# Optimization experiments

Hardware: AMD Instinct MI355X
Metric: run time of the kernel (lower is better)

The kernel has to match this reference:

```python
import jax, jax.numpy as jnp
import numpy as np

B, M, K, D = 16384, 16, 256, 64
T = 1.0


def setup_inputs() -> dict:
    key = jax.random.key(0)
    k1, k2 = jax.random.split(key)
    x = jax.random.normal(k1, (B, M, D), dtype=jnp.float32)
    # nn.init.normal_(self.center, std=0.01)
    center = jax.random.normal(k2, (M, K, D), dtype=jnp.float32) * 0.01
    return {"x": x, "center": center}


def _forward(x, center):
    # x: [B, M, D]; center: [M, K, D]
    x1 = jax.lax.stop_gradient(x)              # x.detach() in the original
    x_sqlen = jnp.sum(x1 * x1, axis=-1)        # [B, M]
    dot = jnp.einsum('mkd,bmd->bmk', center, x1)  # bmm(center, x1) -> [B, M, K]
    c_sqlen = jnp.sum(center * center, axis=-1)   # [M, K]
    dist = c_sqlen[None, :, :] - 2.0 * dot + x_sqlen[:, :, None]  # [B, M, K]
    dist = -jnp.sqrt(dist)
    # softargmax with straight-through estimator
    y_soft = jax.nn.softmax(dist / T, axis=-1)
    label = jnp.argmax(y_soft, axis=-1, keepdims=True)            # [B, M, 1]
    y_hard = jax.nn.one_hot(label[..., 0], K, dtype=dist.dtype)   # [B, M, K]
    assign = y_hard - jax.lax.stop_gradient(y_soft) + y_soft
    # reconstruction: bmm(assign^T(M,B,K), center(M,K,D)) -> [B, M, D]
    recon = jnp.einsum('bmk,mkd->bmd', assign, center)
    return recon, center, label


def reference(x, center):
    return _forward(x, center)
```

## Files before the change

### kernel.cpp

```cpp
#include <hip/hip_runtime.h>
#include <stdint.h>
#include <math.h>

#define B_TOT 16384
#define M_TOT 16
#define K_TOT 256
#define D_TOT 64
#define ROWS_PB 256
#define THREADS 512
#define NCHUNK (B_TOT / ROWS_PB)
#define CAP 2048
#define XERRF 0.0160f
#define CBIG  0.22f
#define SLACK 5.0e-5f

typedef unsigned long long ull;
typedef __attribute__((ext_vector_type(8))) short short8;
typedef __attribute__((ext_vector_type(4))) float f32x4;
typedef __attribute__((ext_vector_type(4))) uint32_t u32x4;

__device__ __forceinline__ uint32_t f32_key(float f) {
  uint32_t u = __float_as_uint(f);
  return (u & 0x80000000u) ? ~u : (u | 0x80000000u);
}
__device__ __forceinline__ ull u64min(ull a, ull b) { return a < b ? a : b; }

__device__ __forceinline__ uint32_t bf16rne(float f) {
  uint32_t u = __float_as_uint(f);
  return (u + 0x7FFFu + ((u >> 16) & 1u)) >> 16;
}
__device__ __forceinline__ uint32_t pack2(float a, float b) {
  return bf16rne(a) | (bf16rne(b) << 16);
}

__device__ __forceinline__ int swz(int row, int c) {
  return row * 128 + ((c * 16) ^ ((row & 7) << 4));
}

#define XLA_SUM64_LANE16(RES, P)                                      \
  do {                                                                \
    float _r[16];                                                     \
    _Pragma("unroll") for (int _j = 0; _j < 16; ++_j) _r[_j] = P(_j); \
    _Pragma("unroll") for (int _mm = 1; _mm < 4; ++_mm)               \
      _Pragma("unroll") for (int _j = 0; _j < 16; ++_j) {             \
        float _q = P(16 * _mm + _j);                                  \
        _r[_j] = _r[_j] + _q;                                         \
      }                                                               \
    float _u[8];                                                      \
    _Pragma("unroll") for (int _j = 0; _j < 8; ++_j) _u[_j] = _r[_j] + _r[_j + 8]; \
    float _v[4];                                                      \
    _Pragma("unroll") for (int _j = 0; _j < 4; ++_j) _v[_j] = _u[_j] + _u[_j + 4]; \
    float _w0 = _v[0] + _v[2];                                        \
    float _w1 = _v[1] + _v[3];                                        \
    RES = _w0 + _w1;                                                  \
  } while (0)

__device__ __forceinline__ ull exact_key_stream(int k, const float* __restrict__ xrow,
                                                const float* __restrict__ crow,
                                                float csq, float x_sq) {
#pragma clang fp contract(off)
#pragma clang fp reassociate(off)
  const float4* cp = reinterpret_cast<const float4*>(crow);
  const float4* xp = reinterpret_cast<const float4*>(xrow);
  float a[4] = {0.f, 0.f, 0.f, 0.f};
#pragma unroll
  for (int it = 0; it < 4; ++it) {
    float cc[16], xx[16];
#pragma unroll
    for (int q = 0; q < 4; ++q) {
      float4 v = cp[4 * it + q];
      cc[4 * q + 0] = v.x; cc[4 * q + 1] = v.y;
      cc[4 * q + 2] = v.z; cc[4 * q + 3] = v.w;
      float4 w = xp[4 * it + q];
      xx[4 * q + 0] = w.x; xx[4 * q + 1] = w.y;
      xx[4 * q + 2] = w.z; xx[4 * q + 3] = w.w;
    }
#pragma unroll
    for (int L = 0; L < 4; ++L) {
      float m3 = cc[12 + L] * xx[12 + L];
      float s3 = m3 + a[L];
      float m2 = cc[8 + L] * xx[8 + L];
      float s2 = m2 + s3;
      float m1 = cc[4 + L] * xx[4 + L];
      float s1 = m1 + s2;
      float m0 = cc[0 + L] * xx[0 + L];
      a[L] = m0 + s1;
    }
  }
  const float dot = (a[0] + a[1]) + (a[2] + a[3]);
  const float two_dot = 2.0f * dot;
  const float d2 = (csq - two_dot) + x_sq;
  const float s = (float)sqrt((double)d2);
  return (((ull)f32_key(s)) << 32) | (unsigned)k;
}

__global__ __launch_bounds__(THREADS, 4) void mkmeans_fwd(
    const float* __restrict__ x, const float* __restrict__ center,
    float* __restrict__ recon, float* __restrict__ outC, float* __restrict__ outL)
{
#pragma clang fp contract(off)
#pragma clang fp reassociate(off)
  __shared__ __align__(16) char s_xb[ROWS_PB * 128];
  __shared__ __align__(16) char s_cb[K_TOT * 128];
  __shared__ __align__(16) float s_csq[K_TOT];
  __shared__ __align__(16) float s_csqrt[K_TOT];
  __shared__ float s_xsq[ROWS_PB];
  __shared__ float s_xnorm[ROWS_PB];
  __shared__ ull s_best[ROWS_PB];
  __shared__ uint32_t s_list[CAP];
  __shared__ int s_nc, s_ovf;

  const int t = threadIdx.x;
  const int l = t & 63;
  const int wv = t >> 6;
  const int g = l >> 4;
  const int j = l & 15;
  const int bi = blockIdx.x;
  const int m = bi & (M_TOT - 1);
  const int chunk = bi >> 4;
  const int b0 = chunk * ROWS_PB;

  const float* cmbase = center + (size_t)m * (K_TOT * D_TOT);

  if (t == 0) { s_nc = 0; s_ovf = 0; }

  if (t < ROWS_PB) {
    const float4* xp = reinterpret_cast<const float4*>(
        x + ((size_t)((b0 + t) * M_TOT + m)) * D_TOT);
    float xf[64];
#pragma unroll
    for (int i = 0; i < 16; ++i) {
      float4 v = xp[i];
      xf[4 * i + 0] = v.x; xf[4 * i + 1] = v.y;
      xf[4 * i + 2] = v.z; xf[4 * i + 3] = v.w;
    }
    float xsq;
#define PX(I) (xf[(I)] * xf[(I)])
    XLA_SUM64_LANE16(xsq, PX);
#undef PX
    s_xsq[t] = xsq;
    s_xnorm[t] = sqrtf(xsq) * 1.00001f + 1e-12f;
#pragma unroll
    for (int c = 0; c < 8; ++c) {
      u32x4 u = {pack2(xf[8 * c + 0], xf[8 * c + 1]),
                 pack2(xf[8 * c + 2], xf[8 * c + 3]),
                 pack2(xf[8 * c + 4], xf[8 * c + 5]),
                 pack2(xf[8 * c + 6], xf[8 * c + 7])};
      *reinterpret_cast<u32x4*>(s_xb + swz(t, c)) = u;
    }
    s_best[t] = ~0ull;
  } else {
    const int tc = t - ROWS_PB;
    const float4* cp = reinterpret_cast<const float4*>(cmbase + (size_t)tc * D_TOT);
    float cf[64];
#pragma unroll
    for (int i = 0; i < 16; ++i) {
      float4 v = cp[i];
      cf[4 * i + 0] = v.x; cf[4 * i + 1] = v.y;
      cf[4 * i + 2] = v.z; cf[4 * i + 3] = v.w;
    }
    float csq;
#define PC(I) (cf[(I)] * cf[(I)])
    XLA_SUM64_LANE16(csq, PC);
#undef PC
    s_csq[tc] = csq;
    s_csqrt[tc] = sqrtf(csq) * 1.00001f + 1e-12f;
#pragma unroll
    for (int c = 0; c < 8; ++c) {
      u32x4 u = {pack2(cf[8 * c + 0], cf[8 * c + 1]),
                 pack2(cf[8 * c + 2], cf[8 * c + 3]),
                 pack2(cf[8 * c + 4], cf[8 * c + 5]),
                 pack2(cf[8 * c + 6], cf[8 * c + 7])};
      *reinterpret_cast<u32x4*>(s_cb + swz(tc, c)) = u;
    }
    if (chunk == 0) {
      float4* dst = reinterpret_cast<float4*>(
          outC + (size_t)m * (K_TOT * D_TOT) + (size_t)tc * D_TOT);
#pragma unroll
      for (int i = 0; i < 16; ++i)
        dst[i] = *reinterpret_cast<const float4*>(&cf[4 * i]);
    }
  }
  __syncthreads();

  const int row0 = wv * 32 + j;
  const int row1 = row0 + 16;
  short8 bfr[2][2];
  float xnorm[2];
#pragma unroll
  for (int rg = 0; rg < 2; ++rg) {
    const int row = rg ? row1 : row0;
#pragma unroll
    for (int ks = 0; ks < 2; ++ks)
      bfr[rg][ks] = *reinterpret_cast<const short8*>(s_xb + swz(row, ks * 4 + g));
    xnorm[rg] = s_xnorm[row];
  }

  float m1[2] = {3.0e38f, 3.0e38f};
#pragma unroll
  for (int T = 0; T < 16; ++T) {
    short8 af[2];
#pragma unroll
    for (int ks = 0; ks < 2; ++ks)
      af[ks] = *reinterpret_cast<const short8*>(s_cb + swz(T * 16 + j, ks * 4 + g));
    const f32x4 cq = *reinterpret_cast<const f32x4*>(&s_csq[T * 16 + g * 4]);
#pragma unroll
    for (int rg = 0; rg < 2; ++rg) {
      f32x4 a = {0.f, 0.f, 0.f, 0.f};
      a = __builtin_amdgcn_mfma_f32_16x16x32_bf16(af[0], bfr[rg][0], a, 0, 0, 0);
      a = __builtin_amdgcn_mfma_f32_16x16x32_bf16(af[1], bfr[rg][1], a, 0, 0, 0);
      const float e0 = fmaf(-2.0f, a[0], cq[0]);
      const float e1 = fmaf(-2.0f, a[1], cq[1]);
      const float e2 = fmaf(-2.0f, a[2], cq[2]);
      const float e3 = fmaf(-2.0f, a[3], cq[3]);
      m1[rg] = fminf(m1[rg], fminf(fminf(e0, e1), fminf(e2, e3)));
    }
  }
  float mthr[2], xbb[2];
#pragma unroll
  for (int rg = 0; rg < 2; ++rg) {
    float v = m1[rg];
    v = fminf(v, __shfl_xor(v, 16, 64));
    v = fminf(v, __shfl_xor(v, 32, 64));
    xbb[rg] = XERRF * xnorm[rg];
    mthr[rg] = v + xbb[rg] * CBIG + SLACK;
  }

#pragma unroll
  for (int T = 0; T < 16; ++T) {
    short8 af[2];
#pragma unroll
    for (int ks = 0; ks < 2; ++ks)
      af[ks] = *reinterpret_cast<const short8*>(s_cb + swz(T * 16 + j, ks * 4 + g));
    const f32x4 cq = *reinterpret_cast<const f32x4*>(&s_csq[T * 16 + g * 4]);
    const f32x4 cs = *reinterpret_cast<const f32x4*>(&s_csqrt[T * 16 + g * 4]);
#pragma unroll
    for (int rg = 0; rg < 2; ++rg) {
      f32x4 a = {0.f, 0.f, 0.f, 0.f};
      a = __builtin_amdgcn_mfma_f32_16x16x32_bf16(af[0], bfr[rg][0], a, 0, 0, 0);
      a = __builtin_amdgcn_mfma_f32_16x16x32_bf16(af[1], bfr[rg][1], a, 0, 0, 0);
      const int row = rg ? row1 : row0;
#pragma unroll
      for (int i = 0; i < 4; ++i) {
        const float am = fmaf(-2.0f, a[i], cq[i]);
        const float thr = fmaf(xbb[rg], cs[i], mthr[rg]);
        if (am <= thr) {
          const int idx = atomicAdd(&s_nc, 1);
          if (idx < CAP)
            s_list[idx] = ((uint32_t)row << 16) | (uint32_t)(T * 16 + g * 4 + i);
          else
            s_ovf = 1;
        }
      }
    }
  }
  __syncthreads();

  if (!s_ovf) {
    const int n = s_nc;
#pragma unroll 1
    for (int i = t; i < n; i += THREADS) {
      const uint32_t e = s_list[i];
      const int row = (int)(e >> 16);
      const int k = (int)(e & 0xffffu);
      const float* xrow = x + ((size_t)((b0 + row) * M_TOT + m)) * D_TOT;
      const float* crow = cmbase + (size_t)k * D_TOT;
      const ull key = exact_key_stream(k, xrow, crow, s_csq[k], s_xsq[row]);
      atomicMin(&s_best[row], key);
    }
  } else if (t < ROWS_PB) {
    const float* xrow = x + ((size_t)((b0 + t) * M_TOT + m)) * D_TOT;
    ull best = ~0ull;
#pragma unroll 1
    for (int k = 0; k < K_TOT; ++k)
      best = u64min(best, exact_key_stream(k, xrow, cmbase + (size_t)k * D_TOT,
                                           s_csq[k], s_xsq[t]));
    s_best[t] = best;
  }
  __syncthreads();

  if (t < ROWS_PB)
    outL[(size_t)(b0 + t) * M_TOT + m] = (float)(uint32_t)(s_best[t] & 0xffffffffull);

  const float4* cm4 = reinterpret_cast<const float4*>(cmbase);
  float4* rec4 = reinterpret_cast<float4*>(recon);
#pragma unroll
  for (int it = 0; it < (ROWS_PB * 16) / THREADS; ++it) {
    const int slot = it * THREADS + t;
    const int row = slot >> 4, ch = slot & 15;
    const int kst = (int)(s_best[row] & 0xffffffffull);
    rec4[((size_t)((b0 + row) * M_TOT + m)) * 16 + ch] = cm4[kst * 16 + ch];
  }
}

extern "C" void kernel_launch(void* const* d_in, const int* in_sizes, int n_in,
                              void* d_out, int out_size, void* d_ws, size_t ws_size,
                              hipStream_t stream) {
  const float* x = (const float*)d_in[0];
  const float* center = (const float*)d_in[1];
  float* recon = (float*)d_out;
  float* outC = recon + (size_t)B_TOT * M_TOT * D_TOT;
  float* outL = outC + (size_t)M_TOT * K_TOT * D_TOT;

  mkmeans_fwd<<<dim3(NCHUNK * M_TOT), dim3(THREADS), 0, stream>>>(x, center, recon, outC, outL);
}
```

Measured before the change: 172.5 us.

## Fuse two MFMA passes into one with online max and candidate bitmasks

Replaces the two-pass candidate search, which ran the bf16 MFMA distance computation twice (once for the minimum, once to collect candidates), with a single pass. That pass seeds the MFMA accumulator with -0.5*||c||^2, tracks a running maximum, and records candidate bits per lane in a 64-bit mask that is reset whenever the maximum jumps. The per-center error bound becomes a uniform bound using the maximum center norm for the block. Staging of x and centers is also restructured to stream in chunks and fuse the outC copy. The looser uniform bound may admit more candidates into the exact rescoring list.

```diff
diff --git a/kernel.cpp b/kernel.cpp
--- a/kernel.cpp
+++ b/kernel.cpp
@@ -11,7 +11,6 @@
 #define NCHUNK (B_TOT / ROWS_PB)
 #define CAP 2048
 #define XERRF 0.0160f
-#define CBIG  0.22f
 #define SLACK 5.0e-5f
 
 typedef unsigned long long ull;
@@ -37,23 +36,19 @@
   return row * 128 + ((c * 16) ^ ((row & 7) << 4));
 }
 
-#define XLA_SUM64_LANE16(RES, P)                                      \
-  do {                                                                \
-    float _r[16];                                                     \
-    _Pragma("unroll") for (int _j = 0; _j < 16; ++_j) _r[_j] = P(_j); \
-    _Pragma("unroll") for (int _mm = 1; _mm < 4; ++_mm)               \
-      _Pragma("unroll") for (int _j = 0; _j < 16; ++_j) {             \
-        float _q = P(16 * _mm + _j);                                  \
-        _r[_j] = _r[_j] + _q;                                         \
-      }                                                               \
-    float _u[8];                                                      \
-    _Pragma("unroll") for (int _j = 0; _j < 8; ++_j) _u[_j] = _r[_j] + _r[_j + 8]; \
-    float _v[4];                                                      \
-    _Pragma("unroll") for (int _j = 0; _j < 4; ++_j) _v[_j] = _u[_j] + _u[_j + 4]; \
-    float _w0 = _v[0] + _v[2];                                        \
-    float _w1 = _v[1] + _v[3];                                        \
-    RES = _w0 + _w1;                                                  \
-  } while (0)
+__device__ __forceinline__ float xla_hsum16(const float* r) {
+#pragma clang fp contract(off)
+#pragma clang fp reassociate(off)
+  float u[8];
+#pragma unroll
+  for (int q = 0; q < 8; ++q) u[q] = r[q] + r[q + 8];
+  float v[4];
+#pragma unroll
+  for (int q = 0; q < 4; ++q) v[q] = u[q] + u[q + 4];
+  float w0 = v[0] + v[2];
+  float w1 = v[1] + v[3];
+  return w0 + w1;
+}
 
 __device__ __forceinline__ ull exact_key_stream(int k, const float* __restrict__ xrow,
                                                 const float* __restrict__ crow,
@@ -103,9 +98,10 @@
   __shared__ __align__(16) char s_xb[ROWS_PB * 128];
   __shared__ __align__(16) char s_cb[K_TOT * 128];
   __shared__ __align__(16) float s_csq[K_TOT];
-  __shared__ __align__(16) float s_csqrt[K_TOT];
+  __shared__ __align__(16) float s_nch[K_TOT];
   __shared__ float s_xsq[ROWS_PB];
   __shared__ float s_xnorm[ROWS_PB];
+  __shared__ float s_cmaxw[4];
   __shared__ ull s_best[ROWS_PB];
   __shared__ uint32_t s_list[CAP];
   __shared__ int s_nc, s_ovf;
@@ -127,130 +123,134 @@
   if (t < ROWS_PB) {
     const float4* xp = reinterpret_cast<const float4*>(
         x + ((size_t)((b0 + t) * M_TOT + m)) * D_TOT);
-    float xf[64];
-#pragma unroll
-    for (int i = 0; i < 16; ++i) {
-      float4 v = xp[i];
-      xf[4 * i + 0] = v.x; xf[4 * i + 1] = v.y;
-      xf[4 * i + 2] = v.z; xf[4 * i + 3] = v.w;
-    }
-    float xsq;
-#define PX(I) (xf[(I)] * xf[(I)])
-    XLA_SUM64_LANE16(xsq, PX);
-#undef PX
+    float r[16];
+#pragma unroll
+    for (int mm = 0; mm < 4; ++mm) {
+      float q[16];
+#pragma unroll
+      for (int qq = 0; qq < 4; ++qq) {
+        float4 v = xp[4 * mm + qq];
+        q[4 * qq + 0] = v.x; q[4 * qq + 1] = v.y;
+        q[4 * qq + 2] = v.z; q[4 * qq + 3] = v.w;
+      }
+#pragma unroll
+      for (int jj = 0; jj < 16; ++jj) {
+        const float p = q[jj] * q[jj];
+        r[jj] = (mm == 0) ? p : (r[jj] + p);
+      }
+#pragma unroll
+      for (int h = 0; h < 2; ++h) {
+        u32x4 u = {pack2(q[8 * h + 0], q[8 * h + 1]),
+                   pack2(q[8 * h + 2], q[8 * h + 3]),
+                   pack2(q[8 * h + 4], q[8 * h + 5]),
+                   pack2(q[8 * h + 6], q[8 * h + 7])};
+        *reinterpret_cast<u32x4*>(s_xb + swz(t, 2 * mm + h)) = u;
+      }
+    }
+    const float xsq = xla_hsum16(r);
     s_xsq[t] = xsq;
     s_xnorm[t] = sqrtf(xsq) * 1.00001f + 1e-12f;
-#pragma unroll
-    for (int c = 0; c < 8; ++c) {
-      u32x4 u = {pack2(xf[8 * c + 0], xf[8 * c + 1]),
-                 pack2(xf[8 * c + 2], xf[8 * c + 3]),
-                 pack2(xf[8 * c + 4], xf[8 * c + 5]),
-                 pack2(xf[8 * c + 6], xf[8 * c + 7])};
-      *reinterpret_cast<u32x4*>(s_xb + swz(t, c)) = u;
-    }
     s_best[t] = ~0ull;
   } else {
     const int tc = t - ROWS_PB;
     const float4* cp = reinterpret_cast<const float4*>(cmbase + (size_t)tc * D_TOT);
-    float cf[64];
-#pragma unroll
-    for (int i = 0; i < 16; ++i) {
-      float4 v = cp[i];
-      cf[4 * i + 0] = v.x; cf[4 * i + 1] = v.y;
-      cf[4 * i + 2] = v.z; cf[4 * i + 3] = v.w;
-    }
-    float csq;
-#define PC(I) (cf[(I)] * cf[(I)])
-    XLA_SUM64_LANE16(csq, PC);
-#undef PC
+    float4* dst = (chunk == 0)
+        ? reinterpret_cast<float4*>(outC + (size_t)m * (K_TOT * D_TOT) + (size_t)tc * D_TOT)
+        : nullptr;
+    float r[16];
+#pragma unroll
+    for (int mm = 0; mm < 4; ++mm) {
+      float q[16];
+#pragma unroll
+      for (int qq = 0; qq < 4; ++qq) {
+        float4 v = cp[4 * mm + qq];
+        if (dst) dst[4 * mm + qq] = v;
+        q[4 * qq + 0] = v.x; q[4 * qq + 1] = v.y;
+        q[4 * qq + 2] = v.z; q[4 * qq + 3] = v.w;
+      }
+#pragma unroll
+      for (int jj = 0; jj < 16; ++jj) {
+        const float p = q[jj] * q[jj];
+        r[jj] = (mm == 0) ? p : (r[jj] + p);
+      }
+#pragma unroll
+      for (int h = 0; h < 2; ++h) {
+        u32x4 u = {pack2(q[8 * h + 0], q[8 * h + 1]),
+                   pack2(q[8 * h + 2], q[8 * h + 3]),
+                   pack2(q[8 * h + 4], q[8 * h + 5]),
+                   pack2(q[8 * h + 6], q[8 * h + 7])};
+        *reinterpret_cast<u32x4*>(s_cb + swz(tc, 2 * mm + h)) = u;
+      }
+    }
+    const float csq = xla_hsum16(r);
     s_csq[tc] = csq;
-    s_csqrt[tc] = sqrtf(csq) * 1.00001f + 1e-12f;
-#pragma unroll
-    for (int c = 0; c < 8; ++c) {
-      u32x4 u = {pack2(cf[8 * c + 0], cf[8 * c + 1]),
-                 pack2(cf[8 * c + 2], cf[8 * c + 3]),
-                 pack2(cf[8 * c + 4], cf[8 * c + 5]),
-                 pack2(cf[8 * c + 6], cf[8 * c + 7])};
-      *reinterpret_cast<u32x4*>(s_cb + swz(tc, c)) = u;
-    }
-    if (chunk == 0) {
-      float4* dst = reinterpret_cast<float4*>(
-          outC + (size_t)m * (K_TOT * D_TOT) + (size_t)tc * D_TOT);
-#pragma unroll
-      for (int i = 0; i < 16; ++i)
-        dst[i] = *reinterpret_cast<const float4*>(&cf[4 * i]);
-    }
+    s_nch[tc] = -0.5f * csq;
+    float cs = sqrtf(csq) * 1.00001f + 1e-12f;
+#pragma unroll
+    for (int off = 1; off < 64; off <<= 1)
+      cs = fmaxf(cs, __shfl_xor(cs, off, 64));
+    if (l == 0) s_cmaxw[wv - 4] = cs;
   }
   __syncthreads();
 
   const int row0 = wv * 32 + j;
   const int row1 = row0 + 16;
   short8 bfr[2][2];
-  float xnorm[2];
 #pragma unroll
   for (int rg = 0; rg < 2; ++rg) {
     const int row = rg ? row1 : row0;
 #pragma unroll
     for (int ks = 0; ks < 2; ++ks)
       bfr[rg][ks] = *reinterpret_cast<const short8*>(s_xb + swz(row, ks * 4 + g));
-    xnorm[rg] = s_xnorm[row];
-  }
-
-  float m1[2] = {3.0e38f, 3.0e38f};
+  }
+  const float cmax = fmaxf(fmaxf(s_cmaxw[0], s_cmaxw[1]),
+                           fmaxf(s_cmaxw[2], s_cmaxw[3]));
+  float Wa[2];
+  Wa[0] = XERRF * s_xnorm[row0] * cmax + 0.5f * SLACK;
+  Wa[1] = XERRF * s_xnorm[row1] * cmax + 0.5f * SLACK;
+
+  float m1[2] = {-3.0e38f, -3.0e38f};
+  ull mk[2] = {0ull, 0ull};
 #pragma unroll
   for (int T = 0; T < 16; ++T) {
-    short8 af[2];
-#pragma unroll
-    for (int ks = 0; ks < 2; ++ks)
-      af[ks] = *reinterpret_cast<const short8*>(s_cb + swz(T * 16 + j, ks * 4 + g));
-    const f32x4 cq = *reinterpret_cast<const f32x4*>(&s_csq[T * 16 + g * 4]);
+    short8 af0 = *reinterpret_cast<const short8*>(s_cb + swz(T * 16 + j, 0 + g));
+    short8 af1 = *reinterpret_cast<const short8*>(s_cb + swz(T * 16 + j, 4 + g));
+    const f32x4 nch = *reinterpret_cast<const f32x4*>(&s_nch[T * 16 + g * 4]);
 #pragma unroll
     for (int rg = 0; rg < 2; ++rg) {
-      f32x4 a = {0.f, 0.f, 0.f, 0.f};
-      a = __builtin_amdgcn_mfma_f32_16x16x32_bf16(af[0], bfr[rg][0], a, 0, 0, 0);
-      a = __builtin_amdgcn_mfma_f32_16x16x32_bf16(af[1], bfr[rg][1], a, 0, 0, 0);
-      const float e0 = fmaf(-2.0f, a[0], cq[0]);
-      const float e1 = fmaf(-2.0f, a[1], cq[1]);
-      const float e2 = fmaf(-2.0f, a[2], cq[2]);
-      const float e3 = fmaf(-2.0f, a[3], cq[3]);
-      m1[rg] = fminf(m1[rg], fminf(fminf(e0, e1), fminf(e2, e3)));
-    }
-  }
-  float mthr[2], xbb[2];
+      f32x4 a = __builtin_amdgcn_mfma_f32_16x16x32_bf16(af0, bfr[rg][0], nch, 0, 0, 0);
+      a = __builtin_amdgcn_mfma_f32_16x16x32_bf16(af1, bfr[rg][1], a, 0, 0, 0);
+      const float tmax = fmaxf(fmaxf(a[0], a[1]), fmaxf(a[2], a[3]));
+      const bool rs = tmax > m1[rg] + Wa[rg];
+      const float m1n = fmaxf(m1[rg], tmax);
+      const float thr = m1n - Wa[rg];
+      uint32_t bits = 0u;
+      bits |= (a[0] >= thr) ? 1u : 0u;
+      bits |= (a[1] >= thr) ? 2u : 0u;
+      bits |= (a[2] >= thr) ? 4u : 0u;
+      bits |= (a[3] >= thr) ? 8u : 0u;
+      mk[rg] = (rs ? 0ull : mk[rg]) | (((ull)bits) << (4 * T));
+      m1[rg] = m1n;
+    }
+  }
+
 #pragma unroll
   for (int rg = 0; rg < 2; ++rg) {
     float v = m1[rg];
-    v = fminf(v, __shfl_xor(v, 16, 64));
-    v = fminf(v, __shfl_xor(v, 32, 64));
-    xbb[rg] = XERRF * xnorm[rg];
-    mthr[rg] = v + xbb[rg] * CBIG + SLACK;
-  }
-
-#pragma unroll
-  for (int T = 0; T < 16; ++T) {
-    short8 af[2];
-#pragma unroll
-    for (int ks = 0; ks < 2; ++ks)
-      af[ks] = *reinterpret_cast<const short8*>(s_cb + swz(T * 16 + j, ks * 4 + g));
-    const f32x4 cq = *reinterpret_cast<const f32x4*>(&s_csq[T * 16 + g * 4]);
-    const f32x4 cs = *reinterpret_cast<const f32x4*>(&s_csqrt[T * 16 + g * 4]);
-#pragma unroll
-    for (int rg = 0; rg < 2; ++rg) {
-      f32x4 a = {0.f, 0.f, 0.f, 0.f};
-      a = __builtin_amdgcn_mfma_f32_16x16x32_bf16(af[0], bfr[rg][0], a, 0, 0, 0);
-      a = __builtin_amdgcn_mfma_f32_16x16x32_bf16(af[1], bfr[rg][1], a, 0, 0, 0);
-      const int row = rg ? row1 : row0;
-#pragma unroll
-      for (int i = 0; i < 4; ++i) {
-        const float am = fmaf(-2.0f, a[i], cq[i]);
-        const float thr = fmaf(xbb[rg], cs[i], mthr[rg]);
-        if (am <= thr) {
-          const int idx = atomicAdd(&s_nc, 1);
-          if (idx < CAP)
-            s_list[idx] = ((uint32_t)row << 16) | (uint32_t)(T * 16 + g * 4 + i);
-          else
-            s_ovf = 1;
-        }
+    v = fmaxf(v, __shfl_xor(v, 16, 64));
+    v = fmaxf(v, __shfl_xor(v, 32, 64));
+    const int row = rg ? row1 : row0;
+    if (m1[rg] >= v - Wa[rg]) {
+      ull msk = mk[rg];
+      while (msk) {
+        const int p = __builtin_ctzll(msk);
+        msk &= msk - 1;
+        const int k = (p >> 2) * 16 + g * 4 + (p & 3);
+        const int idx = atomicAdd(&s_nc, 1);
+        if (idx < CAP)
+          s_list[idx] = ((uint32_t)row << 16) | (uint32_t)k;
+        else
+          s_ovf = 1;
       }
     }
   }
```

New measurement: 211.2 us. 1.22x slower.
